# Optimization experiments

Hardware: AMD Instinct MI355X
Metric: run time of the kernel (lower is better)

## Reference

```python
import jax, jax.numpy as jnp
import numpy as np

E = 2048        # embed_dim
HQ = 32         # num_query_heads
HKV = 8         # num_kv_heads
HD = E // HQ    # head_dim = 64
G = HQ // HKV   # queries per kv head = 4
B, T = 2, 2048


def setup_inputs() -> dict:
    key = jax.random.key(0)
    kx, kq, kkv, ko = jax.random.split(key, 4)
    s = 1.0 / np.sqrt(E)
    x = jax.random.normal(kx, (B, T, E), dtype=jnp.float32)
    Wq = jax.random.normal(kq, (E, E), dtype=jnp.float32) * s          # torch Linear weight (out,in)
    Wkv = jax.random.normal(kkv, (2 * HKV * HD, E), dtype=jnp.float32) * s
    Wo = jax.random.normal(ko, (E, E), dtype=jnp.float32) * s
    return {"x": x, "Wq": Wq, "Wkv": Wkv, "Wo": Wo}


def reference(x, Wq, Wkv, Wo):
    Bx, Tx, C = x.shape
    scale = 1.0 / np.sqrt(HD)
    # projections (torch Linear: y = x @ W.T)
    q = x @ Wq.T                                   # (B,T,E)
    kv = x @ Wkv.T                                 # (B,T,2*HKV*HD)
    k, v = jnp.split(kv, 2, axis=-1)               # each (B,T,HKV*HD)
    # grouped layout: q -> (B,HKV,G,T,HD); k,v -> (B,HKV,T,HD)
    q = q.reshape(Bx, Tx, HKV, G, HD).transpose(0, 2, 3, 1, 4)
    k = k.reshape(Bx, Tx, HKV, HD).transpose(0, 2, 1, 3)
    v = v.reshape(Bx, Tx, HKV, HD).transpose(0, 2, 1, 3)
    # scores: equivalent to repeat_interleave of K over query-head groups
    att = jnp.einsum('bhgtd,bhsd->bhgts', q, k) * scale   # (B,HKV,G,T,T)
    causal = jnp.triu(jnp.ones((Tx, Tx), dtype=bool), k=1)
    att = jnp.where(causal, -jnp.inf, att)
    att = jax.nn.softmax(att, axis=-1)
    out = jnp.einsum('bhgts,bhsd->bhgtd', att, v)          # (B,HKV,G,T,HD)
    out = out.transpose(0, 3, 1, 2, 4).reshape(Bx, Tx, C)  # (B,T,E)
    return out @ Wo.T
```

## Files before the change

kernel.cpp:

```cpp
#include <hip/hip_runtime.h>
#include <hip/hip_bf16.h>
#include <math.h>

#define GQA_B   2
#define GQA_T   2048
#define GQA_E   2048
#define GQA_HQ  32
#define GQA_HKV 8
#define GQA_HD  64
#define GQA_EKV 1024
#define GQA_M   (GQA_B * GQA_T)

typedef short  bf16x8 __attribute__((ext_vector_type(8)));
typedef float  f32x4  __attribute__((ext_vector_type(4)));

#define GLDS16(gsrc, ldst)                                                 \
  __builtin_amdgcn_global_load_lds(                                       \
      (const __attribute__((address_space(1))) void*)(gsrc),              \
      (__attribute__((address_space(3))) void*)(ldst), 16, 0, 0)

__device__ __forceinline__ ushort f2b(float f) {
  union { float f; unsigned u; } c; c.f = f;
  unsigned u = c.u;
  u += 0x7fffu + ((u >> 16) & 1u);
  return (ushort)(u >> 16);
}

__global__ __launch_bounds__(256) void cvt_f32_bf16(
    const float* __restrict__ src, ushort* __restrict__ dst, int n4) {
  int i = blockIdx.x * blockDim.x + threadIdx.x;
  const int stride = gridDim.x * blockDim.x;
  for (; i < n4; i += stride) {
    float4 v = *(const float4*)(src + (size_t)i * 4);
    ushort4 o;
    o.x = f2b(v.x); o.y = f2b(v.y); o.z = f2b(v.z); o.w = f2b(v.w);
    *(ushort4*)(dst + (size_t)i * 4) = o;
  }
}

__device__ __forceinline__ void store_out(ushort* p, float v) { *p = f2b(v); }
__device__ __forceinline__ void store_out(float* p, float v)  { *p = v; }

template <typename CT>
__global__ __launch_bounds__(256) void gemm_nt_bf16(
    const ushort* __restrict__ A, const ushort* __restrict__ B,
    CT* __restrict__ C, int M, int N, int K) {
  __shared__ __align__(16) ushort As[128 * 32];
  __shared__ __align__(16) ushort Bs[128 * 32];
  const int tid = threadIdx.x;
  const int l  = tid & 63;
  const int w  = tid >> 6;
  const int lm = l & 15;
  const int lg = l >> 4;
  const int wm = w & 1;
  const int wn = w >> 1;
  const int bm = blockIdx.y * 128;
  const int bn = blockIdx.x * 128;

  const int srow = w * 32 + (l >> 2);
  const int scol = (l & 3) * 8;
  const ushort* Ag = A + (size_t)(bm + srow) * K + scol;
  const ushort* Bg = B + (size_t)(bn + srow) * K + scol;
  char* ldsA = (char*)As + w * 2048;
  char* ldsB = (char*)Bs + w * 2048;

  f32x4 acc[4][4];
#pragma unroll
  for (int i = 0; i < 4; ++i)
#pragma unroll
    for (int j = 0; j < 4; ++j)
#pragma unroll
      for (int r = 0; r < 4; ++r) acc[i][j][r] = 0.f;

  for (int k0 = 0; k0 < K; k0 += 32) {
    GLDS16(Ag + k0,                  ldsA);
    GLDS16(Ag + (size_t)16 * K + k0, ldsA + 1024);
    GLDS16(Bg + k0,                  ldsB);
    GLDS16(Bg + (size_t)16 * K + k0, ldsB + 1024);
    __syncthreads();

    bf16x8 af[4], bfr[4];
#pragma unroll
    for (int mf = 0; mf < 4; ++mf)
      af[mf] = *(const bf16x8*)(As + (wm * 64 + mf * 16 + lm) * 32 + lg * 8);
#pragma unroll
    for (int nf = 0; nf < 4; ++nf)
      bfr[nf] = *(const bf16x8*)(Bs + (wn * 64 + nf * 16 + lm) * 32 + lg * 8);
#pragma unroll
    for (int mf = 0; mf < 4; ++mf)
#pragma unroll
      for (int nf = 0; nf < 4; ++nf)
        acc[mf][nf] = __builtin_amdgcn_mfma_f32_16x16x32_bf16(
            af[mf], bfr[nf], acc[mf][nf], 0, 0, 0);
    __syncthreads();
  }

#pragma unroll
  for (int mf = 0; mf < 4; ++mf)
#pragma unroll
    for (int nf = 0; nf < 4; ++nf)
#pragma unroll
      for (int r = 0; r < 4; ++r) {
        const int row = bm + wm * 64 + mf * 16 + lg * 4 + r;
        const int col = bn + wn * 64 + nf * 16 + lm;
        store_out(C + (size_t)row * N + col, acc[mf][nf][r]);
      }
}

__global__ __launch_bounds__(256) void gqa_attn_mfma(
    const ushort* __restrict__ Q, const ushort* __restrict__ KV,
    ushort* __restrict__ Oat) {
  const int T = GQA_T, EQ = GQA_E, EKV = GQA_EKV;
  const int qt  = (int)gridDim.x - 1 - (int)blockIdx.x;
  const int qt0 = qt * 64;
  const int hq  = blockIdx.y;
  const int b   = blockIdx.z;
  const int hkv = hq >> 2;

  __shared__ __align__(16) ushort Ks[64 * 64];
  __shared__ __align__(16) ushort Vt[64 * 64];
  __shared__ __align__(16) ushort Ps[4 * 16 * 64];

  const int tid = threadIdx.x;
  const int w  = tid >> 6;
  const int l  = tid & 63;
  const int lm = l & 15;
  const int lg = l >> 4;

  const size_t qrow = ((size_t)b * T + qt0 + 16 * w + lm) * EQ + hq * 64;
  const bf16x8 qa0 = *(const bf16x8*)(Q + qrow + lg * 8);
  const bf16x8 qa1 = *(const bf16x8*)(Q + qrow + 32 + lg * 8);

  f32x4 oacc[4];
#pragma unroll
  for (int nd = 0; nd < 4; ++nd)
#pragma unroll
    for (int r = 0; r < 4; ++r) oacc[nd][r] = 0.f;
  float m2 = -INFINITY, lsum = 0.f;
  const float SCL2 = 0.125f * 1.44269504088896f;

  const size_t kvbase = (size_t)b * T * EKV + hkv * 64;

  const int k_key  = w * 8 + (l >> 3);
  const int k_srcd = (((l & 7) ^ (l >> 3)) * 8);
  char* KsB = (char*)Ks;
  char* VtB = (char*)Vt;
  char* PsB = (char*)Ps + w * 2048;
  char* ldsK0 = KsB + w * 1024;
  char* ldsK1 = KsB + (4 + w) * 1024;
  const int pswz = (lm & 7) << 4;

  const int nt = qt + 1;
  for (int t = 0; t < nt; ++t) {
    const int s0 = t * 64;
    const ushort* kg0 = KV + kvbase + (size_t)(s0 + k_key) * EKV + k_srcd;
    int4 vr0 = *(const int4*)(KV + kvbase + 512 + (size_t)(s0 + l) * EKV + w * 8);
    int4 vr1 = *(const int4*)(KV + kvbase + 512 + (size_t)(s0 + l) * EKV + 32 + w * 8);
    __syncthreads();
    GLDS16(kg0,                       ldsK0);
    GLDS16(kg0 + (size_t)32 * EKV,    ldsK1);
    {
      union { int4 v; ushort u[8]; } a, bq;
      a.v = vr0; bq.v = vr1;
#pragma unroll
      for (int j = 0; j < 8; ++j) {
        const int d0 = w * 8 + j;
        *(ushort*)(VtB + d0 * 128 + ((2 * l) ^ ((d0 & 7) << 4))) = a.u[j];
        const int d1 = 32 + w * 8 + j;
        *(ushort*)(VtB + d1 * 128 + ((2 * l) ^ ((d1 & 7) << 4))) = bq.u[j];
      }
    }
    __syncthreads();

    f32x4 sacc[4];
#pragma unroll
    for (int nf = 0; nf < 4; ++nf)
#pragma unroll
      for (int r = 0; r < 4; ++r) sacc[nf][r] = 0.f;
#pragma unroll
    for (int nf = 0; nf < 4; ++nf) {
      const int krow = nf * 16 + lm;
      const int swz = (krow & 7) << 4;
      bf16x8 kb0 = *(const bf16x8*)(KsB + krow * 128 + ((lg * 16) ^ swz));
      bf16x8 kb1 = *(const bf16x8*)(KsB + krow * 128 + ((64 + lg * 16) ^ swz));
      sacc[nf] = __builtin_amdgcn_mfma_f32_16x16x32_bf16(kb0, qa0, sacc[nf], 0, 0, 0);
      sacc[nf] = __builtin_amdgcn_mfma_f32_16x16x32_bf16(kb1, qa1, sacc[nf], 0, 0, 0);
    }

    const int qg = qt0 + 16 * w + lm;
    if (t == nt - 1) {
#pragma unroll
      for (int nf = 0; nf < 4; ++nf)
#pragma unroll
        for (int r = 0; r < 4; ++r) {
          const int sg = s0 + nf * 16 + lg * 4 + r;
          const float sv = sacc[nf][r] * SCL2;
          sacc[nf][r] = (sg <= qg) ? sv : -INFINITY;
        }
    } else {
#pragma unroll
      for (int nf = 0; nf < 4; ++nf)
#pragma unroll
        for (int r = 0; r < 4; ++r) sacc[nf][r] *= SCL2;
    }

    float mt = -INFINITY;
#pragma unroll
    for (int nf = 0; nf < 4; ++nf)
#pragma unroll
      for (int r = 0; r < 4; ++r) mt = fmaxf(mt, sacc[nf][r]);
    mt = fmaxf(mt, __shfl_xor(mt, 16));
    mt = fmaxf(mt, __shfl_xor(mt, 32));
    const float mnew = fmaxf(m2, mt);
    const float alpha = exp2f(m2 - mnew);
    m2 = mnew;
    float ssum = 0.f;
#pragma unroll
    for (int nf = 0; nf < 4; ++nf)
#pragma unroll
      for (int r = 0; r < 4; ++r) {
        const float p = exp2f(sacc[nf][r] - mnew);
        sacc[nf][r] = p;
        ssum += p;
      }
    ssum += __shfl_xor(ssum, 16);
    ssum += __shfl_xor(ssum, 32);
    lsum = lsum * alpha + ssum;

    float ar[4];
#pragma unroll
    for (int r = 0; r < 4; ++r) ar[r] = __shfl(alpha, lg * 4 + r);
#pragma unroll
    for (int nd = 0; nd < 4; ++nd)
#pragma unroll
      for (int r = 0; r < 4; ++r) oacc[nd][r] *= ar[r];

#pragma unroll
    for (int nf = 0; nf < 4; ++nf) {
      union { uint2 v; __hip_bfloat162 h[2]; } pk;
      pk.h[0] = __float22bfloat162_rn(make_float2(sacc[nf][0], sacc[nf][1]));
      pk.h[1] = __float22bfloat162_rn(make_float2(sacc[nf][2], sacc[nf][3]));
      *(uint2*)(PsB + lm * 128 + ((nf * 32 + lg * 8) ^ pswz)) = pk.v;
    }

    {
      bf16x8 pa0 = *(const bf16x8*)(PsB + lm * 128 + ((lg * 16) ^ pswz));
      bf16x8 pa1 = *(const bf16x8*)(PsB + lm * 128 + ((64 + lg * 16) ^ pswz));
#pragma unroll
      for (int nd = 0; nd < 4; ++nd) {
        const int vrow = nd * 16 + lm;
        const int vswz = (vrow & 7) << 4;
        bf16x8 vb0 = *(const bf16x8*)(VtB + vrow * 128 + ((lg * 16) ^ vswz));
        bf16x8 vb1 = *(const bf16x8*)(VtB + vrow * 128 + ((64 + lg * 16) ^ vswz));
        oacc[nd] = __builtin_amdgcn_mfma_f32_16x16x32_bf16(pa0, vb0, oacc[nd], 0, 0, 0);
        oacc[nd] = __builtin_amdgcn_mfma_f32_16x16x32_bf16(pa1, vb1, oacc[nd], 0, 0, 0);
      }
    }
  }

  const float inv_own = 1.f / lsum;
  float ir[4];
#pragma unroll
  for (int r = 0; r < 4; ++r) ir[r] = __shfl(inv_own, lg * 4 + r);
  const size_t ob = ((size_t)b * T + qt0 + 16 * w + lg * 4) * EQ + hq * 64 + lm;
#pragma unroll
  for (int nd = 0; nd < 4; ++nd)
#pragma unroll
    for (int r = 0; r < 4; ++r)
      Oat[ob + (size_t)r * EQ + nd * 16] = f2b(oacc[nd][r] * ir[r]);
}

extern "C" void kernel_launch(void* const* d_in, const int* in_sizes, int n_in,
                              void* d_out, int out_size, void* d_ws, size_t ws_size,
                              hipStream_t stream) {
  const float* x   = (const float*)d_in[0];
  const float* Wq  = (const float*)d_in[1];
  const float* Wkv = (const float*)d_in[2];
  const float* Wo  = (const float*)d_in[3];
  float* out = (float*)d_out;

  ushort* xb   = (ushort*)d_ws;
  ushort* wqb  = xb   + (size_t)GQA_M * GQA_E;
  ushort* wkvb = wqb  + (size_t)GQA_E * GQA_E;
  ushort* wob  = wkvb + (size_t)GQA_EKV * GQA_E;
  ushort* qb   = wob  + (size_t)GQA_E * GQA_E;
  ushort* kvb  = qb   + (size_t)GQA_M * GQA_E;
  ushort* attb = kvb  + (size_t)GQA_M * GQA_EKV;

  cvt_f32_bf16<<<2048, 256, 0, stream>>>(x,   xb,   GQA_M * GQA_E / 4);
  cvt_f32_bf16<<<1024, 256, 0, stream>>>(Wq,  wqb,  GQA_E * GQA_E / 4);
  cvt_f32_bf16<<<512,  256, 0, stream>>>(Wkv, wkvb, GQA_EKV * GQA_E / 4);
  cvt_f32_bf16<<<1024, 256, 0, stream>>>(Wo,  wob,  GQA_E * GQA_E / 4);

  gemm_nt_bf16<ushort><<<dim3(GQA_E / 128, GQA_M / 128), 256, 0, stream>>>(
      xb, wqb, qb, GQA_M, GQA_E, GQA_E);
  gemm_nt_bf16<ushort><<<dim3(GQA_EKV / 128, GQA_M / 128), 256, 0, stream>>>(
      xb, wkvb, kvb, GQA_M, GQA_EKV, GQA_E);
  gqa_attn_mfma<<<dim3(GQA_T / 64, GQA_HQ, GQA_B), 256, 0, stream>>>(
      qb, kvb, attb);
  gemm_nt_bf16<float><<<dim3(GQA_E / 128, GQA_M / 128), 256, 0, stream>>>(
      attb, wob, out, GQA_M, GQA_E, GQA_E);
}
```

Measured before the change: 460.7 us.

## Double-buffer LDS tiles in GEMM and attention to overlap loads with MFMA

Both the projection GEMM and the attention kernel now use two LDS buffers. The next K-slice or KV tile is prefetched into the alternate buffer while MFMAs run on the current one, and each loop iteration has a single barrier instead of two. The attention kernel also folds the softmax scale into the exp2 argument with an fma rather than scaling every score up front. The cost is double the LDS footprint, which may lower occupancy, plus extra registers to hold the prefetched V tile.

Result: faster. 422.5 us (-8.3%).

```diff
diff --git a/kernel.cpp b/kernel.cpp
--- a/kernel.cpp
+++ b/kernel.cpp
@@ -45,8 +45,8 @@
 __global__ __launch_bounds__(256) void gemm_nt_bf16(
     const ushort* __restrict__ A, const ushort* __restrict__ B,
     CT* __restrict__ C, int M, int N, int K) {
-  __shared__ __align__(16) ushort As[128 * 32];
-  __shared__ __align__(16) ushort Bs[128 * 32];
+  __shared__ __align__(16) ushort As[2 * 128 * 32];
+  __shared__ __align__(16) ushort Bs[2 * 128 * 32];
   const int tid = threadIdx.x;
   const int l  = tid & 63;
   const int w  = tid >> 6;
@@ -61,8 +61,8 @@
   const int scol = (l & 3) * 8;
   const ushort* Ag = A + (size_t)(bm + srow) * K + scol;
   const ushort* Bg = B + (size_t)(bn + srow) * K + scol;
-  char* ldsA = (char*)As + w * 2048;
-  char* ldsB = (char*)Bs + w * 2048;
+  char* ldsAw = (char*)As + w * 2048;
+  char* ldsBw = (char*)Bs + w * 2048;
 
   f32x4 acc[4][4];
 #pragma unroll
@@ -72,20 +72,33 @@
 #pragma unroll
       for (int r = 0; r < 4; ++r) acc[i][j][r] = 0.f;
 
-  for (int k0 = 0; k0 < K; k0 += 32) {
-    GLDS16(Ag + k0,                  ldsA);
-    GLDS16(Ag + (size_t)16 * K + k0, ldsA + 1024);
-    GLDS16(Bg + k0,                  ldsB);
-    GLDS16(Bg + (size_t)16 * K + k0, ldsB + 1024);
-    __syncthreads();
-
+  const int nk = K >> 5;
+  GLDS16(Ag,                  ldsAw);
+  GLDS16(Ag + (size_t)16 * K, ldsAw + 1024);
+  GLDS16(Bg,                  ldsBw);
+  GLDS16(Bg + (size_t)16 * K, ldsBw + 1024);
+  __syncthreads();
+
+  int cur = 0;
+  for (int ks = 0; ks < nk; ++ks) {
+    if (ks + 1 < nk) {
+      const size_t k0 = (size_t)(ks + 1) * 32;
+      char* la = ldsAw + (cur ^ 1) * 8192;
+      char* lb = ldsBw + (cur ^ 1) * 8192;
+      GLDS16(Ag + k0,                  la);
+      GLDS16(Ag + (size_t)16 * K + k0, la + 1024);
+      GLDS16(Bg + k0,                  lb);
+      GLDS16(Bg + (size_t)16 * K + k0, lb + 1024);
+    }
+    const ushort* Ac = As + cur * 4096;
+    const ushort* Bc = Bs + cur * 4096;
     bf16x8 af[4], bfr[4];
 #pragma unroll
     for (int mf = 0; mf < 4; ++mf)
-      af[mf] = *(const bf16x8*)(As + (wm * 64 + mf * 16 + lm) * 32 + lg * 8);
-#pragma unroll
-    for (int nf = 0; nf < 4; ++nf)
-      bfr[nf] = *(const bf16x8*)(Bs + (wn * 64 + nf * 16 + lm) * 32 + lg * 8);
+      af[mf] = *(const bf16x8*)(Ac + (wm * 64 + mf * 16 + lm) * 32 + lg * 8);
+#pragma unroll
+    for (int nf = 0; nf < 4; ++nf)
+      bfr[nf] = *(const bf16x8*)(Bc + (wn * 64 + nf * 16 + lm) * 32 + lg * 8);
 #pragma unroll
     for (int mf = 0; mf < 4; ++mf)
 #pragma unroll
@@ -93,6 +106,7 @@
         acc[mf][nf] = __builtin_amdgcn_mfma_f32_16x16x32_bf16(
             af[mf], bfr[nf], acc[mf][nf], 0, 0, 0);
     __syncthreads();
+    cur ^= 1;
   }
 
 #pragma unroll
@@ -117,8 +131,8 @@
   const int b   = blockIdx.z;
   const int hkv = hq >> 2;
 
-  __shared__ __align__(16) ushort Ks[64 * 64];
-  __shared__ __align__(16) ushort Vt[64 * 64];
+  __shared__ __align__(16) ushort Ks[2 * 64 * 64];
+  __shared__ __align__(16) ushort Vt[2 * 64 * 64];
   __shared__ __align__(16) ushort Ps[4 * 16 * 64];
 
   const int tid = threadIdx.x;
@@ -143,34 +157,46 @@
 
   const int k_key  = w * 8 + (l >> 3);
   const int k_srcd = (((l & 7) ^ (l >> 3)) * 8);
-  char* KsB = (char*)Ks;
-  char* VtB = (char*)Vt;
   char* PsB = (char*)Ps + w * 2048;
-  char* ldsK0 = KsB + w * 1024;
-  char* ldsK1 = KsB + (4 + w) * 1024;
   const int pswz = (lm & 7) << 4;
+  const size_t vgbase = kvbase + 512 + (size_t)l * EKV + w * 8;
 
   const int nt = qt + 1;
+
+  {
+    const ushort* kg = KV + kvbase + (size_t)k_key * EKV + k_srcd;
+    GLDS16(kg,                    (char*)Ks + w * 1024);
+    GLDS16(kg + (size_t)32 * EKV, (char*)Ks + (4 + w) * 1024);
+    int4 v0 = *(const int4*)(KV + vgbase);
+    int4 v1 = *(const int4*)(KV + vgbase + 32);
+    union { int4 v; ushort u[8]; } a, bq;
+    a.v = v0; bq.v = v1;
+#pragma unroll
+    for (int j = 0; j < 8; ++j) {
+      const int d0 = w * 8 + j;
+      *(ushort*)((char*)Vt + d0 * 128 + ((2 * l) ^ ((d0 & 7) << 4))) = a.u[j];
+      const int d1 = 32 + w * 8 + j;
+      *(ushort*)((char*)Vt + d1 * 128 + ((2 * l) ^ ((d1 & 7) << 4))) = bq.u[j];
+    }
+  }
+  __syncthreads();
+
+  int cur = 0;
   for (int t = 0; t < nt; ++t) {
     const int s0 = t * 64;
-    const ushort* kg0 = KV + kvbase + (size_t)(s0 + k_key) * EKV + k_srcd;
-    int4 vr0 = *(const int4*)(KV + kvbase + 512 + (size_t)(s0 + l) * EKV + w * 8);
-    int4 vr1 = *(const int4*)(KV + kvbase + 512 + (size_t)(s0 + l) * EKV + 32 + w * 8);
-    __syncthreads();
-    GLDS16(kg0,                       ldsK0);
-    GLDS16(kg0 + (size_t)32 * EKV,    ldsK1);
-    {
-      union { int4 v; ushort u[8]; } a, bq;
-      a.v = vr0; bq.v = vr1;
-#pragma unroll
-      for (int j = 0; j < 8; ++j) {
-        const int d0 = w * 8 + j;
-        *(ushort*)(VtB + d0 * 128 + ((2 * l) ^ ((d0 & 7) << 4))) = a.u[j];
-        const int d1 = 32 + w * 8 + j;
-        *(ushort*)(VtB + d1 * 128 + ((2 * l) ^ ((d1 & 7) << 4))) = bq.u[j];
-      }
-    }
-    __syncthreads();
+    const bool pf = (t + 1 < nt);
+    int4 nv0, nv1;
+    if (pf) {
+      const size_t s1 = (size_t)(t + 1) * 64;
+      nv0 = *(const int4*)(KV + vgbase + s1 * EKV);
+      nv1 = *(const int4*)(KV + vgbase + s1 * EKV + 32);
+      const ushort* kg = KV + kvbase + (s1 + k_key) * EKV + k_srcd;
+      char* kb = (char*)Ks + (cur ^ 1) * 8192;
+      GLDS16(kg,                    kb + w * 1024);
+      GLDS16(kg + (size_t)32 * EKV, kb + (4 + w) * 1024);
+    }
+    const char* KsB = (const char*)Ks + cur * 8192;
+    const char* VtB = (const char*)Vt + cur * 8192;
 
     f32x4 sacc[4];
 #pragma unroll
@@ -194,14 +220,8 @@
 #pragma unroll
         for (int r = 0; r < 4; ++r) {
           const int sg = s0 + nf * 16 + lg * 4 + r;
-          const float sv = sacc[nf][r] * SCL2;
-          sacc[nf][r] = (sg <= qg) ? sv : -INFINITY;
+          if (sg > qg) sacc[nf][r] = -INFINITY;
         }
-    } else {
-#pragma unroll
-      for (int nf = 0; nf < 4; ++nf)
-#pragma unroll
-        for (int r = 0; r < 4; ++r) sacc[nf][r] *= SCL2;
     }
 
     float mt = -INFINITY;
@@ -211,7 +231,7 @@
       for (int r = 0; r < 4; ++r) mt = fmaxf(mt, sacc[nf][r]);
     mt = fmaxf(mt, __shfl_xor(mt, 16));
     mt = fmaxf(mt, __shfl_xor(mt, 32));
-    const float mnew = fmaxf(m2, mt);
+    const float mnew = fmaxf(m2, mt * SCL2);
     const float alpha = exp2f(m2 - mnew);
     m2 = mnew;
     float ssum = 0.f;
@@ -219,7 +239,7 @@
     for (int nf = 0; nf < 4; ++nf)
 #pragma unroll
       for (int r = 0; r < 4; ++r) {
-        const float p = exp2f(sacc[nf][r] - mnew);
+        const float p = exp2f(fmaf(sacc[nf][r], SCL2, -mnew));
         sacc[nf][r] = p;
         ssum += p;
       }
@@ -256,6 +276,21 @@
         oacc[nd] = __builtin_amdgcn_mfma_f32_16x16x32_bf16(pa1, vb1, oacc[nd], 0, 0, 0);
       }
     }
+
+    if (pf) {
+      char* vb = (char*)Vt + (cur ^ 1) * 8192;
+      union { int4 v; ushort u[8]; } a, bq;
+      a.v = nv0; bq.v = nv1;
+#pragma unroll
+      for (int j = 0; j < 8; ++j) {
+        const int d0 = w * 8 + j;
+        *(ushort*)(vb + d0 * 128 + ((2 * l) ^ ((d0 & 7) << 4))) = a.u[j];
+        const int d1 = 32 + w * 8 + j;
+        *(ushort*)(vb + d1 * 128 + ((2 * l) ^ ((d1 & 7) << 4))) = bq.u[j];
+      }
+    }
+    __syncthreads();
+    cur ^= 1;
   }
 
   const float inv_own = 1.f / lsum;
```
